# Kernel optimization log

Measured on AMD Instinct MI355X. Metric: run time of the kernel, lower is better.

Reference implementation:

```python
import jax, jax.numpy as jnp
import numpy as np

OUT_DIM = 64
N_NODES = 50000
N_EDGES = 1000000


def setup_inputs() -> dict:
    key = jax.random.key(0)
    k1, k2, k3, k4, k5, k6 = jax.random.split(key, 6)
    return {
        "G_h": jax.random.normal(k1, (N_NODES, OUT_DIM), dtype=jnp.float32),
        "K_h": jax.random.normal(k2, (N_NODES, OUT_DIM), dtype=jnp.float32),
        "Q_h": jax.random.normal(k3, (N_NODES, OUT_DIM), dtype=jnp.float32),
        "V_h": jax.random.normal(k4, (N_NODES, 1, OUT_DIM), dtype=jnp.float32),
        "src": jax.random.randint(k5, (N_EDGES,), 0, N_NODES, dtype=jnp.int64),
        "dst": jax.random.randint(k6, (N_EDGES,), 0, N_NODES, dtype=jnp.int64),
    }


def reference(G_h, K_h, Q_h, V_h, src, dst):
    inv_sqrt_d = 1.0 / np.sqrt(OUT_DIM).astype(np.float32)
    # edge-wise gather of node features
    diff = G_h[src] - G_h[dst]                                   # [E, D]
    dist = -jnp.sqrt(jnp.sum(diff * diff, axis=-1) + 1e-6)       # [E]
    distance = jnp.exp(jnp.clip(dist * inv_sqrt_d, -5.0, 5.0))   # [E]
    score = jnp.sum(K_h[src] * Q_h[dst], axis=-1)                # [E]
    score_e = jnp.exp(jnp.clip(score * inv_sqrt_d, -5.0, 5.0))   # [E]
    weight = (score_e * distance)[:, None, None]                 # [E,1,1]
    v1_h = weight * V_h[src]                                     # [E,1,D]
    return v1_h
```

## Files before the change

kernel.cpp:

```cpp
#include <hip/hip_runtime.h>
#include <math.h>

typedef float f32x4 __attribute__((ext_vector_type(4)));

#define MAXNB 256
#define BSHIFT 8
#define UNROLL 8


__global__ void zero_kernel(int* p, int n) {
    int i = blockIdx.x * blockDim.x + threadIdx.x;
    if (i < n) p[i] = 0;
}

__global__ __launch_bounds__(256) void hist_kernel(
    const int* __restrict__ src, int nE, int nb, int* __restrict__ counts)
{
    __shared__ int lc[MAXNB];
    for (int i = threadIdx.x; i < nb; i += blockDim.x) lc[i] = 0;
    __syncthreads();
    for (int e = blockIdx.x * blockDim.x + threadIdx.x; e < nE;
         e += gridDim.x * blockDim.x)
        atomicAdd(&lc[src[e] >> BSHIFT], 1);
    __syncthreads();
    for (int i = threadIdx.x; i < nb; i += blockDim.x) {
        int c = lc[i];
        if (c) atomicAdd(&counts[i], c);
    }
}

__global__ __launch_bounds__(256) void scan_kernel(
    const int* __restrict__ counts, int nb, int* __restrict__ cursor)
{
    __shared__ int buf[MAXNB];
    int t = threadIdx.x;
    int v = (t < nb) ? counts[t] : 0;
    buf[t] = v;
    __syncthreads();
    #pragma unroll
    for (int off = 1; off < MAXNB; off <<= 1) {
        int x = (t >= off) ? buf[t - off] : 0;
        __syncthreads();
        buf[t] += x;
        __syncthreads();
    }
    if (t < nb) cursor[t] = buf[t] - v;
}

__global__ __launch_bounds__(256) void scatter_kernel(
    const int* __restrict__ src, const int* __restrict__ dst, int nE, int nb,
    int* __restrict__ cursor, int* __restrict__ perm,
    int* __restrict__ ssrc, int* __restrict__ sdst)
{
    __shared__ int lc[MAXNB];
    __shared__ int lb[MAXNB];
    const int chunkSize = blockDim.x * UNROLL;
    for (int chunk = blockIdx.x * chunkSize; chunk < nE;
         chunk += gridDim.x * chunkSize) {
        for (int i = threadIdx.x; i < nb; i += blockDim.x) lc[i] = 0;
        __syncthreads();
        int myb[UNROLL], myoff[UNROLL], mys[UNROLL], myd[UNROLL];
        #pragma unroll
        for (int u = 0; u < UNROLL; u++) {
            int e = chunk + u * blockDim.x + threadIdx.x;
            if (e < nE) {
                int s = src[e];
                mys[u] = s; myd[u] = dst[e];
                myb[u] = s >> BSHIFT;
                myoff[u] = atomicAdd(&lc[myb[u]], 1);
            } else myb[u] = -1;
        }
        __syncthreads();
        for (int i = threadIdx.x; i < nb; i += blockDim.x) {
            int c = lc[i];
            lb[i] = c ? atomicAdd(&cursor[i], c) : 0;
        }
        __syncthreads();
        #pragma unroll
        for (int u = 0; u < UNROLL; u++) {
            if (myb[u] >= 0) {
                int pos = lb[myb[u]] + myoff[u];
                int e = chunk + u * blockDim.x + threadIdx.x;
                perm[pos] = e; ssrc[pos] = mys[u]; sdst[pos] = myd[u];
            }
        }
        __syncthreads();
    }
}

__global__ __launch_bounds__(256) void edge_message_kernel(
    const float* __restrict__ G,
    const float* __restrict__ K,
    const float* __restrict__ Q,
    const float* __restrict__ V,
    const int* __restrict__ perm,
    const int* __restrict__ ssrc,
    const int* __restrict__ sdst,
    float* __restrict__ out,
    int nE)
{
    const int tid  = threadIdx.x;
    const int lane = tid & 63;
    const int grp  = lane >> 4;
    const int sub  = lane & 15;
    const int wavesPerBlock = blockDim.x >> 6;
    const int waveId = blockIdx.x * wavesPerBlock + (tid >> 6);
    const int waveStride = gridDim.x * wavesPerBlock;

    const f32x4* __restrict__ G4 = (const f32x4*)G;
    const f32x4* __restrict__ K4 = (const f32x4*)K;
    const f32x4* __restrict__ Q4 = (const f32x4*)Q;
    const f32x4* __restrict__ V4 = (const f32x4*)V;
    f32x4* __restrict__ out4 = (f32x4*)out;

    const float inv_sqrt_d = 0.125f;
    const int last = nE - 1;

    for (int i0 = waveId * 4; i0 < nE; i0 += waveStride * 4) {
        const int i = i0 + grp;
        const bool valid = (i < nE);
        const int ic = valid ? i : last;

        const int s = ssrc[ic];
        const int d = sdst[ic];
        const int o = perm[ic];

        const f32x4 gs = G4[s * 16 + sub];
        const f32x4 gd = G4[d * 16 + sub];
        const f32x4 ks = K4[s * 16 + sub];
        const f32x4 qd = Q4[d * 16 + sub];
        const f32x4 vs = V4[s * 16 + sub];

        const f32x4 df = gs - gd;
        const f32x4 kq = ks * qd;
        float a = df.x * df.x + df.y * df.y + df.z * df.z + df.w * df.w;
        float b = kq.x + kq.y + kq.z + kq.w;

        #pragma unroll
        for (int off = 8; off > 0; off >>= 1) {
            a += __shfl_xor(a, off, 64);
            b += __shfl_xor(b, off, 64);
        }

        float t1 = -sqrtf(a + 1e-6f) * inv_sqrt_d;
        t1 = fminf(fmaxf(t1, -5.0f), 5.0f);
        float t2 = b * inv_sqrt_d;
        t2 = fminf(fmaxf(t2, -5.0f), 5.0f);
        const float w = __expf(t1 + t2);

        if (valid) {
            __builtin_nontemporal_store(w * vs, &out4[(size_t)o * 16 + sub]);
        }
    }
}

extern "C" void kernel_launch(void* const* d_in, const int* in_sizes, int n_in,
                              void* d_out, int out_size, void* d_ws, size_t ws_size,
                              hipStream_t stream)
{
    const float* G   = (const float*)d_in[0];
    const float* K   = (const float*)d_in[1];
    const float* Q   = (const float*)d_in[2];
    const float* V   = (const float*)d_in[3];
    const int*   src = (const int*)d_in[4];
    const int*   dst = (const int*)d_in[5];
    float* out = (float*)d_out;

    const int nE = in_sizes[4];
    const int nNodes = in_sizes[0] / 64;
    const int nb = (nNodes + ((1 << BSHIFT) - 1)) >> BSHIFT;

    int* counts = (int*)d_ws;
    int* cursor = counts + 256;
    int* perm   = cursor + 256;
    int* ssrc   = perm + nE;
    int* sdst   = ssrc + nE;

    zero_kernel<<<2, 256, 0, stream>>>(counts, 512);
    hist_kernel<<<256, 256, 0, stream>>>(src, nE, nb, counts);
    scan_kernel<<<1, 256, 0, stream>>>(counts, nb, cursor);
    {
        const int chunk = 256 * UNROLL;
        int grid = (nE + chunk - 1) / chunk;
        scatter_kernel<<<grid, 256, 0, stream>>>(src, dst, nE, nb,
                                                 cursor, perm, ssrc, sdst);
    }
    {
        const int block = 256;
        const int edgesPerBlock = (block / 64) * 4;
        int grid = (nE + edgesPerBlock - 1) / edgesPerBlock;
        if (grid > 2048) grid = 2048;
        edge_message_kernel<<<grid, block, 0, stream>>>(G, K, Q, V,
                                                        perm, ssrc, sdst, out, nE);
    }
}
```

Before: 442.7 us.

## Pack sorted edge indices into int2 and give each block a contiguous XCD-aware chunk

The scatter now writes a single int2 per edge, holding src and dst packed as 16-bit halves plus the original edge id, in place of three separate int arrays. The message kernel reads one 8-byte record per edge. Each block now handles a contiguous range of the sorted edges, and block indices are remapped so that consecutive chunks land on the same XCD, which should improve L2 reuse of the gathered node rows. Packing into 16 bits assumes node ids below 65536, which holds for 50000 nodes but will silently break for larger graphs.

```diff
diff --git a/kernel.cpp b/kernel.cpp
--- a/kernel.cpp
+++ b/kernel.cpp
@@ -49,8 +49,7 @@
 
 __global__ __launch_bounds__(256) void scatter_kernel(
     const int* __restrict__ src, const int* __restrict__ dst, int nE, int nb,
-    int* __restrict__ cursor, int* __restrict__ perm,
-    int* __restrict__ ssrc, int* __restrict__ sdst)
+    int* __restrict__ cursor, int2* __restrict__ eidx)
 {
     __shared__ int lc[MAXNB];
     __shared__ int lb[MAXNB];
@@ -59,13 +58,13 @@
          chunk += gridDim.x * chunkSize) {
         for (int i = threadIdx.x; i < nb; i += blockDim.x) lc[i] = 0;
         __syncthreads();
-        int myb[UNROLL], myoff[UNROLL], mys[UNROLL], myd[UNROLL];
+        int myb[UNROLL], myoff[UNROLL], pack[UNROLL];
         #pragma unroll
         for (int u = 0; u < UNROLL; u++) {
             int e = chunk + u * blockDim.x + threadIdx.x;
             if (e < nE) {
                 int s = src[e];
-                mys[u] = s; myd[u] = dst[e];
+                pack[u] = s | (dst[e] << 16);
                 myb[u] = s >> BSHIFT;
                 myoff[u] = atomicAdd(&lc[myb[u]], 1);
             } else myb[u] = -1;
@@ -81,7 +80,7 @@
             if (myb[u] >= 0) {
                 int pos = lb[myb[u]] + myoff[u];
                 int e = chunk + u * blockDim.x + threadIdx.x;
-                perm[pos] = e; ssrc[pos] = mys[u]; sdst[pos] = myd[u];
+                eidx[pos] = make_int2(pack[u], e);
             }
         }
         __syncthreads();
@@ -93,19 +92,19 @@
     const float* __restrict__ K,
     const float* __restrict__ Q,
     const float* __restrict__ V,
-    const int* __restrict__ perm,
-    const int* __restrict__ ssrc,
-    const int* __restrict__ sdst,
+    const int2* __restrict__ eidx,
     float* __restrict__ out,
     int nE)
 {
     const int tid  = threadIdx.x;
-    const int lane = tid & 63;
-    const int grp  = lane >> 4;
-    const int sub  = lane & 15;
-    const int wavesPerBlock = blockDim.x >> 6;
-    const int waveId = blockIdx.x * wavesPerBlock + (tid >> 6);
-    const int waveStride = gridDim.x * wavesPerBlock;
+    const int slot = tid >> 4;
+    const int sub  = tid & 15;
+
+    const int nx = gridDim.x >> 3;
+    const int chunkIdx = (blockIdx.x & 7) * nx + (blockIdx.x >> 3);
+    const int perBlock = (nE + gridDim.x - 1) / gridDim.x;
+    const int start = chunkIdx * perBlock;
+    const int end   = min(start + perBlock, nE);
 
     const f32x4* __restrict__ G4 = (const f32x4*)G;
     const f32x4* __restrict__ K4 = (const f32x4*)K;
@@ -114,16 +113,17 @@
     f32x4* __restrict__ out4 = (f32x4*)out;
 
     const float inv_sqrt_d = 0.125f;
-    const int last = nE - 1;
 
-    for (int i0 = waveId * 4; i0 < nE; i0 += waveStride * 4) {
-        const int i = i0 + grp;
-        const bool valid = (i < nE);
-        const int ic = valid ? i : last;
+    for (int i0 = start; i0 < end; i0 += 16) {
+        const int i = i0 + slot;
+        const bool valid = (i < end);
+        const int ic = valid ? i : (end - 1);
 
-        const int s = ssrc[ic];
-        const int d = sdst[ic];
-        const int o = perm[ic];
+        const int2 rec = eidx[ic];
+        const unsigned u = (unsigned)rec.x;
+        const int s = (int)(u & 0xFFFFu);
+        const int d = (int)(u >> 16);
+        const int o = rec.y;
 
         const f32x4 gs = G4[s * 16 + sub];
         const f32x4 gd = G4[d * 16 + sub];
@@ -172,9 +172,7 @@
 
     int* counts = (int*)d_ws;
     int* cursor = counts + 256;
-    int* perm   = cursor + 256;
-    int* ssrc   = perm + nE;
-    int* sdst   = ssrc + nE;
+    int2* eidx  = (int2*)(counts + 512);
 
     zero_kernel<<<2, 256, 0, stream>>>(counts, 512);
     hist_kernel<<<256, 256, 0, stream>>>(src, nE, nb, counts);
@@ -182,15 +180,10 @@
     {
         const int chunk = 256 * UNROLL;
         int grid = (nE + chunk - 1) / chunk;
-        scatter_kernel<<<grid, 256, 0, stream>>>(src, dst, nE, nb,
-                                                 cursor, perm, ssrc, sdst);
+        scatter_kernel<<<grid, 256, 0, stream>>>(src, dst, nE, nb, cursor, eidx);
     }
     {
-        const int block = 256;
-        const int edgesPerBlock = (block / 64) * 4;
-        int grid = (nE + edgesPerBlock - 1) / edgesPerBlock;
-        if (grid > 2048) grid = 2048;
-        edge_message_kernel<<<grid, block, 0, stream>>>(G, K, Q, V,
-                                                        perm, ssrc, sdst, out, nE);
+        int grid = 2048;
+        edge_message_kernel<<<grid, 256, 0, stream>>>(G, K, Q, V, eidx, out, nE);
     }
 }
```

New measurement: 433.0 us. 1.02x faster.
